# Kernel optimization log

Measured on AMD Instinct MI355X. Metric: run time of the kernel, lower is better.

The kernel has to match this reference:

```python
import jax, jax.numpy as jnp
import numpy as np

B, S, I = 16, 512, 64
D, H, L, F = 512, 8, 6, 2048
MAX_REL = 32
EPS = 1e-5


def setup_inputs() -> dict:
    key = jax.random.key(0)
    ks = jax.random.split(key, 16)
    sc = 0.02
    inp = {
        "x": jax.random.normal(ks[0], (B, S, I), dtype=jnp.float32),
        "in_W": jax.random.normal(ks[1], (I, D), dtype=jnp.float32) * sc,
        "in_b": jnp.zeros((D,), jnp.float32),
        "rel_emb": jax.random.normal(ks[2], (2 * MAX_REL + 1, D), dtype=jnp.float32) * sc,
        "qkvo_W": jax.random.normal(ks[3], (L, 4, D, D), dtype=jnp.float32) * sc,
        "qkvo_b": jnp.zeros((L, 4, D), jnp.float32),
        "ln_g": jnp.ones((L, 2, D), jnp.float32),
        "ln_b": jnp.zeros((L, 2, D), jnp.float32),
        "ff_W1": jax.random.normal(ks[4], (L, D, F), dtype=jnp.float32) * sc,
        "ff_b1": jnp.zeros((L, F), jnp.float32),
        "ff_W2": jax.random.normal(ks[5], (L, F, D), dtype=jnp.float32) * sc,
        "ff_b2": jnp.zeros((L, D), jnp.float32),
        "out_W": jax.random.normal(ks[6], (D, 1), dtype=jnp.float32) * sc,
        "out_b": jnp.zeros((1,), jnp.float32),
    }
    return inp


def _layernorm(x, g, b):
    mu = jnp.mean(x, axis=-1, keepdims=True)
    var = jnp.mean((x - mu) ** 2, axis=-1, keepdims=True)
    return (x - mu) * jax.lax.rsqrt(var + EPS) * g + b


def reference(x, in_W, in_b, rel_emb, qkvo_W, qkvo_b, ln_g, ln_b, ff_W1, ff_b1, ff_W2, ff_b2, out_W, out_b):
    b, s, _ = x.shape
    dk = D // H
    h = x @ in_W + in_b  # (B,S,D)
    # relative positional encoding: mean over query axis of gathered embeddings
    pos = jnp.arange(s)
    rel = jnp.clip(pos[:, None] - pos[None, :], -MAX_REL, MAX_REL) + MAX_REL  # (S,S)
    rp = rel_emb[rel]  # (S,S,D)
    h = h + rp.mean(axis=0)[None]  # broadcast over batch

    def layer(h, p):
        Wqkvo, bqkvo, g, bl, W1, b1, W2, b2 = p
        def proj(i):
            return (h @ Wqkvo[i] + bqkvo[i]).reshape(b, s, H, dk).transpose(0, 2, 1, 3)
        q, k, v = proj(0), proj(1), proj(2)  # (B,H,S,dk)
        scores = jnp.einsum("bhqd,bhkd->bhqk", q, k) / jnp.sqrt(jnp.float32(dk))
        attn = jax.nn.softmax(scores, axis=-1)
        ctx = jnp.einsum("bhqk,bhkd->bhqd", attn, v)
        ctx = ctx.transpose(0, 2, 1, 3).reshape(b, s, D)
        ao = ctx @ Wqkvo[3] + bqkvo[3]
        h1 = _layernorm(h + ao, g[0], bl[0])
        ff = jax.nn.relu(h1 @ W1 + b1) @ W2 + b2
        h2 = _layernorm(h1 + ff, g[1], bl[1])
        return h2, None

    h, _ = jax.lax.scan(layer, h, (qkvo_W, qkvo_b, ln_g, ln_b, ff_W1, ff_b1, ff_W2, ff_b2))
    out = h @ out_W + out_b  # (B,S,1)
    return out
```

## Files before the change

kernel.cpp:

```cpp
#include <hip/hip_runtime.h>
#include <math.h>

#define B 16
#define S 512
#define IN 64
#define D 512
#define H 8
#define DK 64
#define L 6
#define F 2048
#define BS (B*S)
#define EPS 1e-5f

typedef short short8 __attribute__((ext_vector_type(8)));
typedef short short4v __attribute__((ext_vector_type(4)));
typedef float floatx4 __attribute__((ext_vector_type(4)));

static __device__ inline short f2bf(float x) {
    unsigned u = __float_as_uint(x);
    unsigned r = (u + 0x7fffu + ((u >> 16) & 1u)) >> 16;
    return (short)r;
}
static __device__ inline float bf2f(short s) {
    return __uint_as_float(((unsigned)(unsigned short)s) << 16);
}

__global__ __launch_bounds__(256) void pe_kernel(const float* __restrict__ rel_emb,
                                                 float* __restrict__ pe) {
    int k = blockIdx.x;
    int d = threadIdx.x;
    float acc0 = 0.f, acc1 = 0.f;
    for (int r = 0; r < 65; ++r) {
        float w;
        if (r == 0)       w = (float)max(0, k - 31);
        else if (r == 64) w = (float)max(0, S - (k + 32));
        else {
            int qpos = k + r - 32;
            w = (qpos >= 0 && qpos < S) ? 1.f : 0.f;
        }
        acc0 += w * rel_emb[r * D + d];
        acc1 += w * rel_emb[r * D + d + 256];
    }
    pe[k * D + d]       = acc0 * (1.f / (float)S);
    pe[k * D + d + 256] = acc1 * (1.f / (float)S);
}

__global__ __launch_bounds__(256) void wtrans_kernel(const float* __restrict__ src,
                                                     short* __restrict__ dst,
                                                     int K, int N) {
    __shared__ float Ls[32][33];
    const int z = blockIdx.z, kb = blockIdx.y, nb = blockIdx.x;
    const int tx = threadIdx.x & 31, ty = threadIdx.x >> 5;
    src += (size_t)z * K * N;
    dst += (size_t)z * K * N;
#pragma unroll
    for (int i = 0; i < 4; ++i)
        Ls[ty + i * 8][tx] = src[(size_t)(kb * 32 + ty + i * 8) * N + nb * 32 + tx];
    __syncthreads();
#pragma unroll
    for (int i = 0; i < 4; ++i) {
        int n = nb * 32 + ty + i * 8;
        dst[(size_t)n * K + kb * 32 + tx] = f2bf(Ls[tx][ty + i * 8]);
    }
}

__global__ __launch_bounds__(256) void cvt_kernel(const float* __restrict__ in,
                                                  short* __restrict__ out) {
    int i = (blockIdx.x * 256 + threadIdx.x) * 4;
    float4 v = *(const float4*)(in + i);
    short4v o;
    o.x = f2bf(v.x); o.y = f2bf(v.y); o.z = f2bf(v.z); o.w = f2bf(v.w);
    *(short4v*)(out + i) = o;
}

__global__ __launch_bounds__(256) void vtrans_kernel(const short* __restrict__ v,
                                                     short* __restrict__ vt) {
    __shared__ short Ls[64 * 72];
    const int bh = blockIdx.y, jt = blockIdx.x * 64;
    const int t = threadIdx.x;
    const int r = t >> 2, cg = t & 3;
    *(short8*)&Ls[r * 72 + cg * 8] =
        *(const short8*)(v + ((size_t)bh * S + jt + r) * DK + cg * 8);
    *(short8*)&Ls[r * 72 + 32 + cg * 8] =
        *(const short8*)(v + ((size_t)bh * S + jt + r) * DK + 32 + cg * 8);
    __syncthreads();
    const int d = t >> 2, sg = t & 3;
    short tmp[16];
#pragma unroll
    for (int i = 0; i < 16; ++i) tmp[i] = Ls[(sg * 16 + i) * 72 + d];
    short* dst = vt + ((size_t)bh * DK + d) * S + jt + sg * 16;
    *(short8*)(dst)     = *(short8*)&tmp[0];
    *(short8*)(dst + 8) = *(short8*)&tmp[8];
}

#define GLL(SRC, DST) __builtin_amdgcn_global_load_lds( \
    (const __attribute__((address_space(1))) void*)(SRC), \
    (__attribute__((address_space(3))) void*)(DST), 16, 0, 0)

__global__ __launch_bounds__(256) void mfma_gemm(
    const short* __restrict__ A, const short* __restrict__ Bt,
    const float* __restrict__ bias, short* __restrict__ Cb,
    int M, int N, int K, int mode,
    const float* __restrict__ pe, long wz, long bz, long cz)
{
    __shared__ short As[128 * 64];
    __shared__ short Bs[128 * 64];

    const int z = blockIdx.z;
    const short* Bz = Bt + (size_t)z * wz;
    const float* bb = bias + (size_t)z * bz;

    const int t = threadIdx.x;
    const int w = t >> 6, lane = t & 63;
    const int wm = w >> 1, wn = w & 1;
    const int ln15 = lane & 15, lq = lane >> 4;
    const int bm = blockIdx.y, bn = blockIdx.x;

    const int ml = lane >> 2;
    const int kb = ((lane & 3) - (ml >> 1)) & 3;
    const short* Ag0 = A  + (size_t)(bm * 128 + w * 16 + ml)       * K + kb * 8;
    const short* Ag1 = A  + (size_t)(bm * 128 + (w + 4) * 16 + ml) * K + kb * 8;
    const short* Bg0 = Bz + (size_t)(bn * 128 + w * 16 + ml)       * K + kb * 8;
    const short* Bg1 = Bz + (size_t)(bn * 128 + (w + 4) * 16 + ml) * K + kb * 8;
    short* A00 = As + (w * 2 + 0) * 512;
    short* A01 = As + (w * 2 + 1) * 512;
    short* A10 = As + ((w + 4) * 2 + 0) * 512;
    short* A11 = As + ((w + 4) * 2 + 1) * 512;
    short* B00 = Bs + (w * 2 + 0) * 512;
    short* B01 = Bs + (w * 2 + 1) * 512;
    short* B10 = Bs + ((w + 4) * 2 + 0) * 512;
    short* B11 = Bs + ((w + 4) * 2 + 1) * 512;

    floatx4 acc[4][4] = {};
    const int slot = ln15 * 4 + ((lq + (ln15 >> 1)) & 3);

    for (int kt = 0; kt < K; kt += 64) {
        __syncthreads();
        GLL(Ag0 + kt,      A00);
        GLL(Ag0 + kt + 32, A01);
        GLL(Ag1 + kt,      A10);
        GLL(Ag1 + kt + 32, A11);
        GLL(Bg0 + kt,      B00);
        GLL(Bg0 + kt + 32, B01);
        GLL(Bg1 + kt,      B10);
        GLL(Bg1 + kt + 32, B11);
        __syncthreads();

#pragma unroll
        for (int p = 0; p < 2; ++p) {
            short8 af[4], bf[4];
#pragma unroll
            for (int mt = 0; mt < 4; ++mt) {
                af[mt] = *(const short8*)&As[(((wm * 4 + mt) * 2 + p) * 64 + slot) * 8];
                bf[mt] = *(const short8*)&Bs[(((wn * 4 + mt) * 2 + p) * 64 + slot) * 8];
            }
#pragma unroll
            for (int mt = 0; mt < 4; ++mt)
#pragma unroll
                for (int nt = 0; nt < 4; ++nt)
                    acc[mt][nt] = __builtin_amdgcn_mfma_f32_16x16x32_bf16(
                        af[mt], bf[nt], acc[mt][nt], 0, 0, 0);
        }
    }

    short* Cbz = Cb + (size_t)z * cz;
#pragma unroll
    for (int mt = 0; mt < 4; ++mt) {
#pragma unroll
        for (int nt = 0; nt < 4; ++nt) {
            const int col = bn * 128 + wn * 64 + nt * 16 + ln15;
            const int row0 = bm * 128 + wm * 64 + mt * 16 + lq * 4;
            const float bc = bb[col];
#pragma unroll
            for (int reg = 0; reg < 4; ++reg) {
                const int r = row0 + reg;
                float v = acc[mt][nt][reg] + bc;
                if (mode == 1) v = fmaxf(v, 0.f);
                else if (mode == 2) v += pe[(size_t)(r & (S - 1)) * D + col];
                if (mode == 3) {
                    const int bi = r >> 9, si = r & (S - 1);
                    const int hh = col >> 6, dd = col & 63;
                    Cbz[(((size_t)(bi * H + hh) * S + si) * DK + dd)] = f2bf(v);
                } else {
                    Cb[(size_t)r * N + col] = f2bf(v);
                }
            }
        }
    }
}

__global__ __launch_bounds__(256) void attn_mfma(
    const short* __restrict__ qg, const short* __restrict__ kg,
    const short* __restrict__ vtg, short* __restrict__ ctx)
{
    __shared__ short Ks[64 * 72];
    __shared__ short Vs[64 * 72];
    __shared__ short Ps[4][16 * 72];

    const int t = threadIdx.x;
    const int w = t >> 6, lane = t & 63;
    const int ln15 = lane & 15, lq = lane >> 4;
    const int bh = blockIdx.y, bi = bh >> 3, hh = bh & 7;
    const int qbase = blockIdx.x * 64 + w * 16;

    short8 qf0, qf1;
    {
        const short* qrow = qg + ((size_t)bh * S + qbase + ln15) * DK;
        qf0 = *(const short8*)(qrow + lq * 8);
        qf1 = *(const short8*)(qrow + 32 + lq * 8);
    }
    floatx4 o[4] = {};
    float mrow[4] = {-1e30f, -1e30f, -1e30f, -1e30f};
    float lrow[4] = {};

    const int sr = t >> 2, scg = t & 3;
    const short* kbase = kg  + (size_t)bh * S * DK;
    const short* vtb   = vtg + (size_t)bh * DK * S;

    for (int jt = 0; jt < S; jt += 64) {
        __syncthreads();
        *(short8*)&Ks[sr * 72 + scg * 8] =
            *(const short8*)(kbase + (size_t)(jt + sr) * DK + scg * 8);
        *(short8*)&Ks[sr * 72 + 32 + scg * 8] =
            *(const short8*)(kbase + (size_t)(jt + sr) * DK + 32 + scg * 8);
        *(short8*)&Vs[sr * 72 + scg * 8] =
            *(const short8*)(vtb + (size_t)sr * S + jt + scg * 8);
        *(short8*)&Vs[sr * 72 + 32 + scg * 8] =
            *(const short8*)(vtb + (size_t)sr * S + jt + 32 + scg * 8);
        __syncthreads();

        floatx4 sc[4];
#pragma unroll
        for (int nt = 0; nt < 4; ++nt) {
            floatx4 s4 = {};
            short8 kf0 = *(const short8*)&Ks[(nt * 16 + ln15) * 72 + lq * 8];
            short8 kf1 = *(const short8*)&Ks[(nt * 16 + ln15) * 72 + 32 + lq * 8];
            s4 = __builtin_amdgcn_mfma_f32_16x16x32_bf16(qf0, kf0, s4, 0, 0, 0);
            s4 = __builtin_amdgcn_mfma_f32_16x16x32_bf16(qf1, kf1, s4, 0, 0, 0);
#pragma unroll
            for (int r = 0; r < 4; ++r) s4[r] *= 0.125f;
            sc[nt] = s4;
        }

        float rmax[4];
#pragma unroll
        for (int r = 0; r < 4; ++r)
            rmax[r] = fmaxf(fmaxf(sc[0][r], sc[1][r]), fmaxf(sc[2][r], sc[3][r]));
#pragma unroll
        for (int off = 1; off < 16; off <<= 1)
#pragma unroll
            for (int r = 0; r < 4; ++r)
                rmax[r] = fmaxf(rmax[r], __shfl_xor(rmax[r], off));

        float mnew[4], alpha[4], psum[4];
#pragma unroll
        for (int r = 0; r < 4; ++r) {
            mnew[r]  = fmaxf(mrow[r], rmax[r]);
            alpha[r] = __expf(mrow[r] - mnew[r]);
            psum[r]  = 0.f;
        }
#pragma unroll
        for (int nt = 0; nt < 4; ++nt)
#pragma unroll
            for (int r = 0; r < 4; ++r) {
                float p = __expf(sc[nt][r] - mnew[r]);
                psum[r] += p;
                Ps[w][(lq * 4 + r) * 72 + nt * 16 + ln15] = f2bf(p);
            }
#pragma unroll
        for (int off = 1; off < 16; off <<= 1)
#pragma unroll
            for (int r = 0; r < 4; ++r)
                psum[r] += __shfl_xor(psum[r], off);
#pragma unroll
        for (int r = 0; r < 4; ++r) {
            lrow[r] = lrow[r] * alpha[r] + psum[r];
            mrow[r] = mnew[r];
        }
#pragma unroll
        for (int dv = 0; dv < 4; ++dv)
#pragma unroll
            for (int r = 0; r < 4; ++r)
                o[dv][r] *= alpha[r];

        short8 pf0 = *(const short8*)&Ps[w][ln15 * 72 + lq * 8];
        short8 pf1 = *(const short8*)&Ps[w][ln15 * 72 + 32 + lq * 8];
#pragma unroll
        for (int dv = 0; dv < 4; ++dv) {
            short8 vf0 = *(const short8*)&Vs[(dv * 16 + ln15) * 72 + lq * 8];
            short8 vf1 = *(const short8*)&Vs[(dv * 16 + ln15) * 72 + 32 + lq * 8];
            o[dv] = __builtin_amdgcn_mfma_f32_16x16x32_bf16(pf0, vf0, o[dv], 0, 0, 0);
            o[dv] = __builtin_amdgcn_mfma_f32_16x16x32_bf16(pf1, vf1, o[dv], 0, 0, 0);
        }
    }

    float inv[4];
#pragma unroll
    for (int r = 0; r < 4; ++r) inv[r] = 1.f / lrow[r];
#pragma unroll
    for (int dv = 0; dv < 4; ++dv)
#pragma unroll
        for (int r = 0; r < 4; ++r) {
            const int s = qbase + lq * 4 + r;
            const int col = hh * DK + dv * 16 + ln15;
            ctx[((size_t)bi * S + s) * D + col] = f2bf(o[dv][r] * inv[r]);
        }
}

__global__ __launch_bounds__(128) void ln_kernel(
    const short* __restrict__ a, const short* __restrict__ bres,
    const float* __restrict__ g, const float* __restrict__ beta,
    short* __restrict__ outb)
{
    const int row = blockIdx.x;
    const int t = threadIdx.x;
    const short4v xa = *(const short4v*)(a    + (size_t)row * D + t * 4);
    const short4v xb = *(const short4v*)(bres + (size_t)row * D + t * 4);
    float x0 = bf2f(xa.x) + bf2f(xb.x), x1 = bf2f(xa.y) + bf2f(xb.y);
    float x2 = bf2f(xa.z) + bf2f(xb.z), x3 = bf2f(xa.w) + bf2f(xb.w);
    float s  = x0 + x1 + x2 + x3;
    float s2 = x0 * x0 + x1 * x1 + x2 * x2 + x3 * x3;
#pragma unroll
    for (int o = 32; o > 0; o >>= 1) {
        s  += __shfl_down(s, o);
        s2 += __shfl_down(s2, o);
    }
    __shared__ float red[2][2];
    const int wave = t >> 6;
    if ((t & 63) == 0) { red[wave][0] = s; red[wave][1] = s2; }
    __syncthreads();
    s  = red[0][0] + red[1][0];
    s2 = red[0][1] + red[1][1];
    const float mu  = s * (1.f / (float)D);
    const float var = s2 * (1.f / (float)D) - mu * mu;
    const float r   = rsqrtf(var + EPS);
    const float4 gg = *(const float4*)(g    + t * 4);
    const float4 bb = *(const float4*)(beta + t * 4);
    short4v ob;
    ob.x = f2bf((x0 - mu) * r * gg.x + bb.x);
    ob.y = f2bf((x1 - mu) * r * gg.y + bb.y);
    ob.z = f2bf((x2 - mu) * r * gg.z + bb.z);
    ob.w = f2bf((x3 - mu) * r * gg.w + bb.w);
    *(short4v*)(outb + (size_t)row * D + t * 4) = ob;
}

__global__ __launch_bounds__(256) void out_kernel(
    const short* __restrict__ h, const float* __restrict__ ow,
    const float* __restrict__ ob, float* __restrict__ out)
{
    const int wave = threadIdx.x >> 6;
    const int lane = threadIdx.x & 63;
    const int row  = blockIdx.x * 4 + wave;
    const short* hp = h + (size_t)row * D;
    float s = 0.f;
#pragma unroll
    for (int u = 0; u < 8; ++u) {
        int d = lane + u * 64;
        s += bf2f(hp[d]) * ow[d];
    }
#pragma unroll
    for (int o = 32; o > 0; o >>= 1) s += __shfl_down(s, o);
    if (lane == 0) out[row] = s + ob[0];
}

extern "C" void kernel_launch(void* const* d_in, const int* in_sizes, int n_in,
                              void* d_out, int out_size, void* d_ws, size_t ws_size,
                              hipStream_t stream) {
    const float* x       = (const float*)d_in[0];
    const float* in_W    = (const float*)d_in[1];
    const float* in_b    = (const float*)d_in[2];
    const float* rel_emb = (const float*)d_in[3];
    const float* qkvo_W  = (const float*)d_in[4];
    const float* qkvo_b  = (const float*)d_in[5];
    const float* ln_g    = (const float*)d_in[6];
    const float* ln_bb   = (const float*)d_in[7];
    const float* ff_W1   = (const float*)d_in[8];
    const float* ff_b1   = (const float*)d_in[9];
    const float* ff_W2   = (const float*)d_in[10];
    const float* ff_b2   = (const float*)d_in[11];
    const float* out_W   = (const float*)d_in[12];
    const float* out_b   = (const float*)d_in[13];
    float* out = (float*)d_out;

    const size_t HSZ = (size_t)BS * D;
    float* pe     = (float*)d_ws;
    short* h_bf   = (short*)(pe + (size_t)S * D);
    short* h1_bf  = h_bf  + HSZ;
    short* tmp_bf = h1_bf + HSZ;
    short* qkv_bf = tmp_bf + HSZ;
    short* xb     = qkv_bf + 4 * HSZ;
    short* wt_qkvo = xb + (size_t)BS * IN;
    short* wt_ff1  = wt_qkvo + (size_t)L * 4 * D * D;
    short* wt_ff2  = wt_ff1  + (size_t)L * D * F;
    short* wt_in   = wt_ff2  + (size_t)L * F * D;

    const size_t CZ = (size_t)B * H * S * DK;
    short* qb = qkv_bf;
    short* kb = qkv_bf + CZ;
    short* vb = qkv_bf + 2 * CZ;
    short* vt = qkv_bf + 3 * CZ;
    short* ctx_bf = vb;
    short* ff1_bf = qkv_bf;

    dim3 blk(256);

    pe_kernel<<<dim3(S), blk, 0, stream>>>(rel_emb, pe);
    cvt_kernel<<<dim3(BS * IN / 1024), blk, 0, stream>>>(x, xb);
    wtrans_kernel<<<dim3(D / 32, IN / 32, 1), blk, 0, stream>>>(in_W, wt_in, IN, D);
    wtrans_kernel<<<dim3(D / 32, D / 32, 4 * L), blk, 0, stream>>>(qkvo_W, wt_qkvo, D, D);
    wtrans_kernel<<<dim3(F / 32, D / 32, L), blk, 0, stream>>>(ff_W1, wt_ff1, D, F);
    wtrans_kernel<<<dim3(D / 32, F / 32, L), blk, 0, stream>>>(ff_W2, wt_ff2, F, D);

    mfma_gemm<<<dim3(D / 128, BS / 128, 1), blk, 0, stream>>>(
        xb, wt_in, in_b, h_bf, BS, D, IN, 2, pe, 0, 0, 0);

    for (int l = 0; l < L; ++l) {
        const float* bl = qkvo_b + (size_t)l * 4 * D;
        mfma_gemm<<<dim3(D / 128, BS / 128, 3), blk, 0, stream>>>(
            h_bf, wt_qkvo + (size_t)l * 4 * D * D, bl, qkv_bf, BS, D, D, 3,
            nullptr, (long)D * D, (long)D, (long)CZ);
        vtrans_kernel<<<dim3(S / 64, B * H), blk, 0, stream>>>(vb, vt);
        attn_mfma<<<dim3(S / 64, B * H), blk, 0, stream>>>(qb, kb, vt, ctx_bf);
        mfma_gemm<<<dim3(D / 128, BS / 128, 1), blk, 0, stream>>>(
            ctx_bf, wt_qkvo + (size_t)(l * 4 + 3) * D * D, bl + 3 * D, tmp_bf,
            BS, D, D, 0, nullptr, 0, 0, 0);
        ln_kernel<<<dim3(BS), dim3(128), 0, stream>>>(
            h_bf, tmp_bf, ln_g + (size_t)l * 2 * D, ln_bb + (size_t)l * 2 * D, h1_bf);
        mfma_gemm<<<dim3(F / 128, BS / 128, 1), blk, 0, stream>>>(
            h1_bf, wt_ff1 + (size_t)l * D * F, ff_b1 + (size_t)l * F, ff1_bf,
            BS, F, D, 1, nullptr, 0, 0, 0);
        mfma_gemm<<<dim3(D / 128, BS / 128, 1), blk, 0, stream>>>(
            ff1_bf, wt_ff2 + (size_t)l * F * D, ff_b2 + (size_t)l * D, tmp_bf,
            BS, D, F, 0, nullptr, 0, 0, 0);
        ln_kernel<<<dim3(BS), dim3(128), 0, stream>>>(
            h1_bf, tmp_bf, ln_g + (size_t)l * 2 * D + D, ln_bb + (size_t)l * 2 * D + D,
            h_bf);
    }

    out_kernel<<<dim3(BS / 4), blk, 0, stream>>>(h_bf, out_W, out_b, out);
}
```

Before: 1.247 ms.

## Double-buffer LDS tiles in the MFMA GEMM with half-depth K steps

Splits the shared-memory A/B tiles into two 32-wide K buffers and prefetches the next K slice via global_load_lds while MFMAs consume the current one. This removes one of the two barriers per iteration and aims to overlap global-to-LDS transfer with matrix math. In exchange the K loop runs twice as many iterations with less compute per barrier. It also relies on the barrier draining the outstanding async loads before each buffer is read.

```diff
diff --git a/kernel.cpp b/kernel.cpp
--- a/kernel.cpp
+++ b/kernel.cpp
@@ -103,8 +103,8 @@
     int M, int N, int K, int mode,
     const float* __restrict__ pe, long wz, long bz, long cz)
 {
-    __shared__ short As[128 * 64];
-    __shared__ short Bs[128 * 64];
+    __shared__ short As[2][128 * 32];
+    __shared__ short Bs[2][128 * 32];
 
     const int z = blockIdx.z;
     const short* Bz = Bt + (size_t)z * wz;
@@ -122,45 +122,39 @@
     const short* Ag1 = A  + (size_t)(bm * 128 + (w + 4) * 16 + ml) * K + kb * 8;
     const short* Bg0 = Bz + (size_t)(bn * 128 + w * 16 + ml)       * K + kb * 8;
     const short* Bg1 = Bz + (size_t)(bn * 128 + (w + 4) * 16 + ml) * K + kb * 8;
-    short* A00 = As + (w * 2 + 0) * 512;
-    short* A01 = As + (w * 2 + 1) * 512;
-    short* A10 = As + ((w + 4) * 2 + 0) * 512;
-    short* A11 = As + ((w + 4) * 2 + 1) * 512;
-    short* B00 = Bs + (w * 2 + 0) * 512;
-    short* B01 = Bs + (w * 2 + 1) * 512;
-    short* B10 = Bs + ((w + 4) * 2 + 0) * 512;
-    short* B11 = Bs + ((w + 4) * 2 + 1) * 512;
+    const int so0 = w * 512, so1 = (w + 4) * 512;
 
     floatx4 acc[4][4] = {};
     const int slot = ln15 * 4 + ((lq + (ln15 >> 1)) & 3);
 
-    for (int kt = 0; kt < K; kt += 64) {
+    GLL(Ag0, &As[0][so0]);
+    GLL(Ag1, &As[0][so1]);
+    GLL(Bg0, &Bs[0][so0]);
+    GLL(Bg1, &Bs[0][so1]);
+
+    int buf = 0;
+    for (int kt = 0; kt < K; kt += 32) {
         __syncthreads();
-        GLL(Ag0 + kt,      A00);
-        GLL(Ag0 + kt + 32, A01);
-        GLL(Ag1 + kt,      A10);
-        GLL(Ag1 + kt + 32, A11);
-        GLL(Bg0 + kt,      B00);
-        GLL(Bg0 + kt + 32, B01);
-        GLL(Bg1 + kt,      B10);
-        GLL(Bg1 + kt + 32, B11);
-        __syncthreads();
-
-#pragma unroll
-        for (int p = 0; p < 2; ++p) {
-            short8 af[4], bf[4];
-#pragma unroll
-            for (int mt = 0; mt < 4; ++mt) {
-                af[mt] = *(const short8*)&As[(((wm * 4 + mt) * 2 + p) * 64 + slot) * 8];
-                bf[mt] = *(const short8*)&Bs[(((wn * 4 + mt) * 2 + p) * 64 + slot) * 8];
-            }
-#pragma unroll
-            for (int mt = 0; mt < 4; ++mt)
-#pragma unroll
-                for (int nt = 0; nt < 4; ++nt)
-                    acc[mt][nt] = __builtin_amdgcn_mfma_f32_16x16x32_bf16(
-                        af[mt], bf[nt], acc[mt][nt], 0, 0, 0);
-        }
+        const int ktn = kt + 32;
+        if (ktn < K) {
+            GLL(Ag0 + ktn, &As[buf ^ 1][so0]);
+            GLL(Ag1 + ktn, &As[buf ^ 1][so1]);
+            GLL(Bg0 + ktn, &Bs[buf ^ 1][so0]);
+            GLL(Bg1 + ktn, &Bs[buf ^ 1][so1]);
+        }
+        short8 af[4], bf[4];
+#pragma unroll
+        for (int mt = 0; mt < 4; ++mt) {
+            af[mt] = *(const short8*)&As[buf][((wm * 4 + mt) * 64 + slot) * 8];
+            bf[mt] = *(const short8*)&Bs[buf][((wn * 4 + mt) * 64 + slot) * 8];
+        }
+#pragma unroll
+        for (int mt = 0; mt < 4; ++mt)
+#pragma unroll
+            for (int nt = 0; nt < 4; ++nt)
+                acc[mt][nt] = __builtin_amdgcn_mfma_f32_16x16x32_bf16(
+                    af[mt], bf[nt], acc[mt][nt], 0, 0, 0);
+        buf ^= 1;
     }
 
     short* Cbz = Cb + (size_t)z * cz;
```

Result: no change. 1.271 ms (+1.9%).
